# Performance work log

Hardware: AMD Instinct MI355X
Metric: run time of the kernel (lower is better)

The kernel has to match this reference:

```python
import jax, jax.numpy as jnp
import numpy as np

EPSILON = 1e-5  # parameters.EPSILON
BN_EPS = 1e-5
N_NODES, N_EDGES, D = 50000, 400000, 128


def batch_norm(x, gamma, beta):
    # BatchNorm1d in training mode: biased batch statistics over dim 0
    m = jnp.mean(x, axis=0)
    v = jnp.var(x, axis=0)
    return (x - m) * jax.lax.rsqrt(v + BN_EPS) * gamma + beta


def setup_inputs() -> dict:
    key = jax.random.key(0)
    ks = jax.random.split(key, 16)
    s = 0.05
    d = D
    inp = {
        "h": jax.random.normal(ks[0], (N_NODES, d), jnp.float32),
        "e": jax.random.normal(ks[1], (N_EDGES, d), jnp.float32),
        "src": jax.random.randint(ks[2], (N_EDGES,), 0, N_NODES, jnp.int32),
        "dst": jax.random.randint(ks[3], (N_EDGES,), 0, N_NODES, jnp.int32),
        # weights stored [in, out]
        "W_emb_node": jax.random.normal(ks[4], (d, d)) * s,
        "W_emb_edge": jax.random.normal(ks[5], (d, d)) * s,
        "W_emb_eta": jax.random.normal(ks[6], (d, d)) * s,
        "Uw": jax.random.normal(ks[7], (d, d)) * s, "Ub": jnp.zeros((d,)),
        "Vw": jax.random.normal(ks[8], (d, d)) * s, "Vb": jnp.zeros((d,)),
        "W1w": jax.random.normal(ks[9], (d, d)) * s, "W1b": jnp.zeros((d,)),
        "W2w": jax.random.normal(ks[10], (d, d)) * s, "W2b": jnp.zeros((d,)),
        "W3w": jax.random.normal(ks[11], (d, d)) * s, "W3b": jnp.zeros((d,)),
        "h_gamma": jnp.ones((d,)), "h_beta": jnp.zeros((d,)),
        "e_gamma": jnp.ones((d,)), "e_beta": jnp.zeros((d,)),
    }
    return inp


def reference(h, e, src, dst, W_emb_node, W_emb_edge, W_emb_eta,
              Uw, Ub, Vw, Vb, W1w, W1b, W2w, W2b, W3w, W3b,
              h_gamma, h_beta, e_gamma, e_beta):
    n_nodes = h.shape[0]
    # node-level linear projections
    h_emb = h @ W_emb_node                 # [N, d]
    Uh = h @ Uw + Ub                       # [N, d]
    Vh = h @ Vw + Vb                       # [N, d]
    W2h = h @ W2w + W2b                    # [N, d]
    W3h = h @ W3w + W3b                    # [N, d]
    # edge-level
    e_emb = e @ W_emb_edge                 # [E, d]
    W1e = e @ W1w + W1b                    # [E, d]
    # edge update: e_ij = emb(e) + ReLU(BN(W1 e + W2 h_src + W3 h_dst))
    pre_e = W1e + W2h[src] + W3h[dst]      # gather [E, d]
    e_new = e_emb + jax.nn.relu(batch_norm(pre_e, e_gamma, e_beta))
    # gate: sigma_ij = embedding_eta(sigmoid(e_ij))
    sigma = jax.nn.sigmoid(e_new) @ W_emb_eta  # [E, d]
    # weighted-sum aggregation to destination nodes
    num = jax.ops.segment_sum(sigma * Vh[src], dst, num_segments=n_nodes)
    den = jax.ops.segment_sum(sigma, dst, num_segments=n_nodes)
    agg = num / (den + EPSILON)            # [N, d]
    h_new = h_emb + jax.nn.relu(batch_norm(Uh + agg, h_gamma, h_beta))
    return (h_new, e_new)
```

## Files before the change

kernel.cpp:

```cpp
#include <hip/hip_runtime.h>
#include <cstdint>
#include <cstddef>
#include <cmath>

#define DD 128

typedef short bf16x8 __attribute__((ext_vector_type(8)));
typedef float f32x4 __attribute__((ext_vector_type(4)));

static __device__ __forceinline__ short f2bf(float f){
  union { float f; uint32_t u; } v; v.f = f;
  uint32_t r = v.u + 0x7FFFu + ((v.u >> 16) & 1u);
  return (short)(r >> 16);
}
static __device__ __forceinline__ float bf2f(short h){
  union { uint32_t u; float f; } v; v.u = ((uint32_t)(uint16_t)h) << 16;
  return v.f;
}
static __device__ __forceinline__ double shfl_xor_f64(double v, int m){
  long long l = __double_as_longlong(v);
  int lo = (int)(l & 0xffffffffLL);
  int hi = (int)((unsigned long long)l >> 32);
  lo = __shfl_xor(lo, m, 64);
  hi = __shfl_xor(hi, m, 64);
  return __longlong_as_double(((long long)hi << 32) | (unsigned long long)(unsigned int)lo);
}

template<int EP>
__global__ __launch_bounds__(256, 2) void fgemm_k(
    const float* __restrict__ X, const float* __restrict__ W,
    const float* __restrict__ bias, float* __restrict__ Y,
    int M, int nTiles,
    const int* __restrict__ src, const int* __restrict__ dst,
    const float* __restrict__ T2, const float* __restrict__ T3,
    const float* __restrict__ mF, const float* __restrict__ rF,
    const float* __restrict__ gammaF, const float* __restrict__ betaF,
    double* __restrict__ eSum, double* __restrict__ eSumSq)
{
  __shared__ float sA[128][68];
  __shared__ float sW[64][128];
  __shared__ double redS[(EP == 1) ? 4 : 1][32][4];
  __shared__ double redQ[(EP == 1) ? 4 : 1][32][4];

  const int tid = threadIdx.x;
  const int tx = tid & 31;
  const int ty = tid >> 5;
  const int c0 = tx * 4;
  const int r0 = ty * 16;
  const int lane = tid & 63, wv = tid >> 6;

  float bias_c[4];
  #pragma unroll
  for (int j = 0; j < 4; ++j) bias_c[j] = bias ? bias[c0 + j] : 0.0f;

  double st_s[4] = {0,0,0,0}, st_q[4] = {0,0,0,0};

  for (int tile = blockIdx.x; tile < nTiles; tile += gridDim.x){
    const int rowBase = tile * 128;
    float acc[16][4];
    #pragma unroll
    for (int r = 0; r < 16; ++r)
      #pragma unroll
      for (int j = 0; j < 4; ++j) acc[r][j] = 0.0f;

    #pragma unroll
    for (int h = 0; h < 2; ++h){
      {
        int kk = ty * 8;
        #pragma unroll
        for (int q = 0; q < 8; ++q)
          *(f32x4*)&sW[kk + q][c0] = *(const f32x4*)&W[(size_t)(h*64 + kk + q) * DD + c0];
      }
      {
        int r = tid >> 1;
        int koff = (tid & 1) * 32;
        int ar = rowBase + r; if (ar >= M) ar = M - 1;
        const float* xp = X + (size_t)ar * DD + h*64 + koff;
        #pragma unroll
        for (int q = 0; q < 8; ++q){
          f32x4 v = *(const f32x4*)(xp + q * 4);
          if (EP == 3){
            #pragma unroll
            for (int j = 0; j < 4; ++j) v[j] = 1.0f / (1.0f + expf(-v[j]));
          }
          *(f32x4*)&sA[r][koff + q * 4] = v;
        }
      }
      __syncthreads();

      #pragma unroll 2
      for (int q = 0; q < 16; ++q){
        f32x4 b0 = *(const f32x4*)&sW[4*q + 0][c0];
        f32x4 b1 = *(const f32x4*)&sW[4*q + 1][c0];
        f32x4 b2 = *(const f32x4*)&sW[4*q + 2][c0];
        f32x4 b3 = *(const f32x4*)&sW[4*q + 3][c0];
        #pragma unroll
        for (int r = 0; r < 16; ++r){
          f32x4 a = *(const f32x4*)&sA[r0 + r][4*q];
          #pragma unroll
          for (int j = 0; j < 4; ++j){
            acc[r][j] = fmaf(a[0], b0[j], acc[r][j]);
            acc[r][j] = fmaf(a[1], b1[j], acc[r][j]);
            acc[r][j] = fmaf(a[2], b2[j], acc[r][j]);
            acc[r][j] = fmaf(a[3], b3[j], acc[r][j]);
          }
        }
      }
      __syncthreads();
    }

    #pragma unroll
    for (int r = 0; r < 16; ++r){
      int row = rowBase + r0 + r;
      if (row < M){
        size_t base = (size_t)row * DD + c0;
        if (EP == 0){
          f32x4 o;
          #pragma unroll
          for (int j = 0; j < 4; ++j) o[j] = acc[r][j] + bias_c[j];
          *(f32x4*)&Y[base] = o;
        } else if (EP == 1){
          int s = src[row], d = dst[row];
          f32x4 t2 = *(const f32x4*)&T2[(size_t)s * DD + c0];
          f32x4 t3 = *(const f32x4*)&T3[(size_t)d * DD + c0];
          f32x4 o;
          #pragma unroll
          for (int j = 0; j < 4; ++j){
            o[j] = ((acc[r][j] + bias_c[j]) + t2[j]) + t3[j];
            st_s[j] += (double)o[j];
            st_q[j] += (double)o[j] * (double)o[j];
          }
          *(f32x4*)&Y[base] = o;
        } else if (EP == 2){
          f32x4 pe = *(const f32x4*)&Y[base];
          f32x4 o;
          #pragma unroll
          for (int j = 0; j < 4; ++j){
            float xm  = pe[j] - mF[c0 + j];
            float t1  = xm * rF[c0 + j];
            float t2v = t1 * gammaF[c0 + j];
            float t3v = t2v + betaF[c0 + j];
            float t = fmaxf(t3v, 0.0f);
            o[j] = acc[r][j] + t;
          }
          *(f32x4*)&Y[base] = o;
        } else {
          f32x4 o;
          #pragma unroll
          for (int j = 0; j < 4; ++j) o[j] = acc[r][j];
          *(f32x4*)&Y[base] = o;
        }
      }
    }
  }

  if (EP == 1){
    #pragma unroll
    for (int j = 0; j < 4; ++j){
      st_s[j] += shfl_xor_f64(st_s[j], 32);
      st_q[j] += shfl_xor_f64(st_q[j], 32);
    }
    if (lane < 32){
      #pragma unroll
      for (int j = 0; j < 4; ++j){ redS[wv][lane][j] = st_s[j]; redQ[wv][lane][j] = st_q[j]; }
    }
    __syncthreads();
    if (tid < 128){
      int txx = tid >> 2, j = tid & 3;
      double s = 0.0, q = 0.0;
      #pragma unroll
      for (int w = 0; w < 4; ++w){ s += redS[w][txx][j]; q += redQ[w][txx][j]; }
      atomicAdd(&eSum[txx*4 + j], s);
      atomicAdd(&eSumSq[txx*4 + j], q);
    }
  }
}

__global__ void hist_k(const int* __restrict__ dst, int NE, int* __restrict__ counts){
  int i = blockIdx.x * blockDim.x + threadIdx.x;
  if (i < NE) atomicAdd(&counts[dst[i]], 1);
}

__global__ __launch_bounds__(1024, 1) void scan_k(const int* __restrict__ counts, int NN,
                                                  int* __restrict__ rowStart, int* __restrict__ cursor){
  __shared__ int part[1024];
  const int T = 1024, t = threadIdx.x;
  const int chunk = (NN + T - 1) / T;
  const int lo = t * chunk;
  const int hi = (lo + chunk < NN) ? lo + chunk : NN;
  int s = 0;
  for (int i = lo; i < hi; ++i) s += counts[i];
  part[t] = s;
  __syncthreads();
  for (int off = 1; off < T; off <<= 1){
    int v = (t >= off) ? part[t - off] : 0;
    __syncthreads();
    part[t] += v;
    __syncthreads();
  }
  int run = (t == 0) ? 0 : part[t - 1];
  for (int i = lo; i < hi; ++i){ rowStart[i] = run; cursor[i] = run; run += counts[i]; }
  if (t == T - 1) rowStart[NN] = run;
}

__global__ void place_k(const int* __restrict__ dst, int NE,
                        int* __restrict__ cursor, int* __restrict__ edgeIdx){
  int i = blockIdx.x * blockDim.x + threadIdx.x;
  if (i < NE){ int p = atomicAdd(&cursor[dst[i]], 1); edgeIdx[p] = i; }
}

__global__ __launch_bounds__(256, 4) void gather_k(
    const float* __restrict__ sigma, const float* __restrict__ Vh,
    const int* __restrict__ rowStart, const int* __restrict__ edgeIdx,
    const int* __restrict__ srcArr,
    const float* __restrict__ Uh, float* __restrict__ preH, int NN)
{
  const int lane = threadIdx.x & 63, wv = threadIdx.x >> 6;
  for (int node = blockIdx.x * 4 + wv; node < NN; node += gridDim.x * 4){
    const int beg = rowStart[node], end = rowStart[node + 1];
    float den0 = 0.f, den1 = 0.f, num0 = 0.f, num1 = 0.f;
    for (int eb = beg; eb < end; eb += 4){
      const int nE = end - eb;
      float sg0[4], sg1[4], vh0[4], vh1[4];
      #pragma unroll
      for (int q = 0; q < 4; ++q){
        if (q < nE){
          int eid = edgeIdx[eb + q];
          int s = srcArr[eid];
          sg0[q] = sigma[(size_t)eid * DD + lane];
          sg1[q] = sigma[(size_t)eid * DD + 64 + lane];
          vh0[q] = Vh[(size_t)s * DD + lane];
          vh1[q] = Vh[(size_t)s * DD + 64 + lane];
        } else { sg0[q] = 0.f; sg1[q] = 0.f; vh0[q] = 0.f; vh1[q] = 0.f; }
      }
      #pragma unroll
      for (int q = 0; q < 4; ++q){
        den0 += sg0[q]; den1 += sg1[q];
        num0 = fmaf(sg0[q], vh0[q], num0);
        num1 = fmaf(sg1[q], vh1[q], num1);
      }
    }
    const size_t b = (size_t)node * DD;
    preH[b + lane]      = Uh[b + lane]      + num0 / (den0 + 1e-5f);
    preH[b + 64 + lane] = Uh[b + 64 + lane] + num1 / (den1 + 1e-5f);
  }
}

__global__ void finalizeE_k(const double* __restrict__ sum, const double* __restrict__ sumsq,
                            double M, float* __restrict__ mF, float* __restrict__ rF)
{
  int c = threadIdx.x;
  double m = sum[c] / M;
  double v = sumsq[c] / M - m * m;
  float vf = (float)v;
  mF[c] = (float)m;
  rF[c] = 1.0f / sqrtf(vf + 1e-5f);
}

__global__ void stats64_k(const float* __restrict__ X, int M,
                          double* __restrict__ sum, double* __restrict__ sumsq)
{
  const int col = threadIdx.x & 127;
  const int half = threadIdx.x >> 7;
  double s = 0.0, q = 0.0;
  for (int r = blockIdx.x * 2 + half; r < M; r += gridDim.x * 2){
    double v = (double)X[(size_t)r * DD + col];
    s += v; q += v * v;
  }
  __shared__ double sS[256], sQ[256];
  sS[threadIdx.x] = s; sQ[threadIdx.x] = q;
  __syncthreads();
  if (half == 0){
    atomicAdd(&sum[col],   sS[col] + sS[col + 128]);
    atomicAdd(&sumsq[col], sQ[col] + sQ[col + 128]);
  }
}

__global__ void finalize64_k(const double* __restrict__ sum, const double* __restrict__ sumsq,
                             double M, const float* __restrict__ gamma, const float* __restrict__ beta,
                             double* __restrict__ scale, double* __restrict__ shift)
{
  int c = threadIdx.x;
  double m = sum[c] / M;
  double var = sumsq[c] / M - m * m;
  double sc = (double)gamma[c] / sqrt(var + 1e-5);
  scale[c] = sc;
  shift[c] = (double)beta[c] - m * sc;
}

__global__ __launch_bounds__(256, 2) void hfinal_mfma_k(
    const float* __restrict__ X, const float* __restrict__ W,
    float* __restrict__ Y, int M, int rowTiles,
    const float* __restrict__ preH,
    const double* __restrict__ hSc, const double* __restrict__ hSh)
{
  const int tid = threadIdx.x;
  const int lane = tid & 63;
  const int wv = tid >> 6;
  const int l15 = lane & 15;
  const int lg = lane >> 4;
  const int colBase = blockIdx.y * 64;

  __shared__ short sW[2][64][136];
  for (int t = tid; t < 64 * 128; t += 256){
    int k = t >> 6, nl = t & 63;
    float w = W[k * DD + colBase + nl];
    short hi = f2bf(w);
    sW[0][nl][k] = hi;
    sW[1][nl][k] = f2bf(w - bf2f(hi));
  }
  __syncthreads();

  bf16x8 Bhi[4][4], Blo[4][4];
  #pragma unroll
  for (int ct = 0; ct < 4; ++ct)
    #pragma unroll
    for (int ks = 0; ks < 4; ++ks){
      Bhi[ct][ks] = *(const bf16x8*)&sW[0][ct*16 + l15][ks*32 + lg*8];
      Blo[ct][ks] = *(const bf16x8*)&sW[1][ct*16 + l15][ks*32 + lg*8];
    }

  for (int rt = blockIdx.x; rt < rowTiles; rt += gridDim.x){
    int arow = rt * 64 + wv * 16 + l15;
    if (arow >= M) arow = M - 1;
    const f32x4* xr = (const f32x4*)(X + (size_t)arow * DD);

    bf16x8 Ahi[4], Alo[4];
    #pragma unroll
    for (int ks = 0; ks < 4; ++ks){
      f32x4 a0 = xr[ks*8 + lg*2];
      f32x4 a1 = xr[ks*8 + lg*2 + 1];
      float av[8];
      #pragma unroll
      for (int j = 0; j < 4; ++j){ av[j] = a0[j]; av[4+j] = a1[j]; }
      #pragma unroll
      for (int j = 0; j < 8; ++j){
        short hi = f2bf(av[j]);
        Ahi[ks][j] = hi;
        Alo[ks][j] = f2bf(av[j] - bf2f(hi));
      }
    }

    f32x4 acc[4];
    #pragma unroll
    for (int ct = 0; ct < 4; ++ct) acc[ct] = (f32x4){0.f, 0.f, 0.f, 0.f};
    #pragma unroll
    for (int ct = 0; ct < 4; ++ct)
      #pragma unroll
      for (int ks = 0; ks < 4; ++ks){
        acc[ct] = __builtin_amdgcn_mfma_f32_16x16x32_bf16(Ahi[ks], Bhi[ct][ks], acc[ct], 0, 0, 0);
        acc[ct] = __builtin_amdgcn_mfma_f32_16x16x32_bf16(Ahi[ks], Blo[ct][ks], acc[ct], 0, 0, 0);
        acc[ct] = __builtin_amdgcn_mfma_f32_16x16x32_bf16(Alo[ks], Bhi[ct][ks], acc[ct], 0, 0, 0);
      }

    const int r0 = rt * 64 + wv * 16 + lg * 4;
    #pragma unroll
    for (int reg = 0; reg < 4; ++reg){
      int r = r0 + reg;
      if (r < M){
        #pragma unroll
        for (int ct = 0; ct < 4; ++ct){
          int c = colBase + ct*16 + l15;
          double t = (double)preH[(size_t)r * DD + c] * hSc[c] + hSh[c];
          float tv = t > 0.0 ? (float)t : 0.0f;
          Y[(size_t)r * DD + c] = acc[ct][reg] + tv;
        }
      }
    }
  }
}

extern "C" void kernel_launch(void* const* d_in, const int* in_sizes, int n_in,
                              void* d_out, int out_size, void* d_ws, size_t ws_size,
                              hipStream_t stream)
{
  const float* h  = (const float*)d_in[0];
  const float* e  = (const float*)d_in[1];
  const int* src  = (const int*)d_in[2];
  const int* dst  = (const int*)d_in[3];
  const float* Wemb_n   = (const float*)d_in[4];
  const float* Wemb_e   = (const float*)d_in[5];
  const float* Wemb_eta = (const float*)d_in[6];
  const float* Uw  = (const float*)d_in[7];  const float* Ub  = (const float*)d_in[8];
  const float* Vw  = (const float*)d_in[9];  const float* Vb  = (const float*)d_in[10];
  const float* W1w = (const float*)d_in[11]; const float* W1b = (const float*)d_in[12];
  const float* W2w = (const float*)d_in[13]; const float* W2b = (const float*)d_in[14];
  const float* W3w = (const float*)d_in[15]; const float* W3b = (const float*)d_in[16];
  const float* h_gamma = (const float*)d_in[17]; const float* h_beta = (const float*)d_in[18];
  const float* e_gamma = (const float*)d_in[19]; const float* e_beta = (const float*)d_in[20];

  const int NN = in_sizes[0] / DD;
  const int NE = in_sizes[2];

  char* wsp = (char*)d_ws;
  float* W2h   = (float*)wsp;  wsp += (size_t)NN * DD * sizeof(float);
  float* W3h   = (float*)wsp;  wsp += (size_t)NN * DD * sizeof(float);
  float* Vh    = (float*)wsp;  wsp += (size_t)NN * DD * sizeof(float);
  float* sigma = (float*)wsp;  wsp += (size_t)NE * DD * sizeof(float);
  double* stats = (double*)wsp; wsp += 6 * DD * sizeof(double);
  double* eSum = stats;        double* eSumSq = stats + DD;
  double* hSum = stats + 2*DD; double* hSumSq = stats + 3*DD;
  double* hScale = stats + 4*DD; double* hShift = stats + 5*DD;
  float* mF = (float*)wsp;   wsp += DD * sizeof(float);
  float* rF = (float*)wsp;   wsp += DD * sizeof(float);
  int* counts   = (int*)wsp; wsp += (size_t)NN * sizeof(int);
  int* rowStart = (int*)wsp; wsp += ((size_t)NN + 1) * sizeof(int);
  int* cursor   = (int*)wsp; wsp += (size_t)NN * sizeof(int);
  int* edgeIdx  = (int*)wsp; wsp += (size_t)NE * sizeof(int);

  float* h_new_out = (float*)d_out;
  float* e_out     = (float*)d_out + (size_t)NN * DD;

  const int tN = (NN + 127) / 128;
  const int tE = (NE + 127) / 128;
  const int rtN64 = (NN + 63) / 64;
  dim3 blk(256);

  hipMemsetAsync(stats, 0, (size_t)4 * DD * sizeof(double), stream);
  hipMemsetAsync(counts, 0, (size_t)NN * sizeof(int), stream);

  hist_k<<<(NE + 255) / 256, blk, 0, stream>>>(dst, NE, counts);
  scan_k<<<1, 1024, 0, stream>>>(counts, NN, rowStart, cursor);
  place_k<<<(NE + 255) / 256, blk, 0, stream>>>(dst, NE, cursor, edgeIdx);

  fgemm_k<0><<<tN, blk, 0, stream>>>(h, Uw, Ub, h_new_out, NN, tN,
      nullptr,nullptr,nullptr,nullptr,nullptr,nullptr,nullptr,nullptr,nullptr,nullptr);
  fgemm_k<0><<<tN, blk, 0, stream>>>(h, Vw, Vb, Vh, NN, tN,
      nullptr,nullptr,nullptr,nullptr,nullptr,nullptr,nullptr,nullptr,nullptr,nullptr);
  fgemm_k<0><<<tN, blk, 0, stream>>>(h, W2w, W2b, W2h, NN, tN,
      nullptr,nullptr,nullptr,nullptr,nullptr,nullptr,nullptr,nullptr,nullptr,nullptr);
  fgemm_k<0><<<tN, blk, 0, stream>>>(h, W3w, W3b, W3h, NN, tN,
      nullptr,nullptr,nullptr,nullptr,nullptr,nullptr,nullptr,nullptr,nullptr,nullptr);

  fgemm_k<1><<<1024, blk, 0, stream>>>(e, W1w, W1b, e_out, NE, tE,
      src, dst, W2h, W3h, nullptr,nullptr,nullptr,nullptr, eSum, eSumSq);

  finalizeE_k<<<1, 128, 0, stream>>>(eSum, eSumSq, (double)NE, mF, rF);

  fgemm_k<2><<<tE, blk, 0, stream>>>(e, Wemb_e, nullptr, e_out, NE, tE,
      nullptr,nullptr,nullptr,nullptr, mF, rF, e_gamma, e_beta, nullptr,nullptr);

  fgemm_k<3><<<tE, blk, 0, stream>>>(e_out, Wemb_eta, nullptr, sigma, NE, tE,
      nullptr,nullptr,nullptr,nullptr,nullptr,nullptr,nullptr,nullptr,nullptr,nullptr);

  gather_k<<<(NN + 3) / 4, blk, 0, stream>>>(sigma, Vh, rowStart, edgeIdx, src,
      h_new_out, h_new_out, NN);

  stats64_k<<<512, blk, 0, stream>>>(h_new_out, NN, hSum, hSumSq);
  finalize64_k<<<1, 128, 0, stream>>>(hSum, hSumSq, (double)NN, h_gamma, h_beta, hScale, hShift);

  hfinal_mfma_k<<<dim3(rtN64, 2), blk, 0, stream>>>(h, Wemb_n, h_new_out, NN, rtN64,
      h_new_out, hScale, hShift);
}
```

Before: 1.223 ms.

## Fuse paired node/edge GEMMs sharing inputs and fold edge BN into sigma GEMM

Node projections are paired into dual-output GEMMs (U+V, W2+W3), so h is read twice instead of four times. The edge W1 and embedding GEMMs now share one pass over e. The edge BN/ReLU/residual epilogue moves into the sigma GEMM's A-tile load, which writes e_new and feeds sigmoid(e_new) straight to the eta GEMM. This removes kernel launches and full passes over the large edge arrays. In exchange the dual kernel holds twice the accumulators, raising register pressure, and the sigma kernel works in place on shared buffers.

```diff
diff --git a/kernel.cpp b/kernel.cpp
--- a/kernel.cpp
+++ b/kernel.cpp
@@ -27,34 +27,156 @@
 }
 
 template<int EP>
-__global__ __launch_bounds__(256, 2) void fgemm_k(
-    const float* __restrict__ X, const float* __restrict__ W,
-    const float* __restrict__ bias, float* __restrict__ Y,
+__global__ __launch_bounds__(256, 2) void dgemm_k(
+    const float* __restrict__ X,
+    const float* __restrict__ W1, const float* __restrict__ b1,
+    const float* __restrict__ W2, const float* __restrict__ b2,
+    float* __restrict__ Y1, float* __restrict__ Y2,
     int M, int nTiles,
     const int* __restrict__ src, const int* __restrict__ dst,
     const float* __restrict__ T2, const float* __restrict__ T3,
+    double* __restrict__ eSum, double* __restrict__ eSumSq)
+{
+  __shared__ float sA[128][36];
+  __shared__ float sW1[32][128];
+  __shared__ float sW2[32][128];
+  __shared__ double redS[(EP == 1) ? 4 : 1][32][4];
+  __shared__ double redQ[(EP == 1) ? 4 : 1][32][4];
+
+  const int tid = threadIdx.x, tx = tid & 31, ty = tid >> 5;
+  const int c0 = tx * 4, r0 = ty * 16;
+  const int lane = tid & 63, wv = tid >> 6;
+
+  float b1c[4], b2c[4];
+  #pragma unroll
+  for (int j = 0; j < 4; ++j){
+    b1c[j] = b1 ? b1[c0 + j] : 0.0f;
+    b2c[j] = b2 ? b2[c0 + j] : 0.0f;
+  }
+  double st_s[4] = {0,0,0,0}, st_q[4] = {0,0,0,0};
+
+  #pragma unroll 1
+  for (int tile = blockIdx.x; tile < nTiles; tile += gridDim.x){
+    const int rowBase = tile * 128;
+    float acc1[16][4], acc2[16][4];
+    #pragma unroll
+    for (int r = 0; r < 16; ++r)
+      #pragma unroll
+      for (int j = 0; j < 4; ++j){ acc1[r][j] = 0.0f; acc2[r][j] = 0.0f; }
+
+    #pragma unroll 1
+    for (int h = 0; h < 4; ++h){
+      #pragma unroll
+      for (int m = 0; m < 4; ++m){
+        int k = ty + 8 * m;
+        *(f32x4*)&sW1[k][c0] = *(const f32x4*)&W1[(size_t)(h*32 + k) * DD + c0];
+        *(f32x4*)&sW2[k][c0] = *(const f32x4*)&W2[(size_t)(h*32 + k) * DD + c0];
+      }
+      {
+        int r = tid >> 1, koff = (tid & 1) * 16;
+        int ar = rowBase + r; if (ar >= M) ar = M - 1;
+        const float* xp = X + (size_t)ar * DD + h*32 + koff;
+        #pragma unroll
+        for (int q = 0; q < 4; ++q)
+          *(f32x4*)&sA[r][koff + q*4] = *(const f32x4*)(xp + q*4);
+      }
+      __syncthreads();
+
+      #pragma unroll
+      for (int q = 0; q < 8; ++q){
+        f32x4 wA0 = *(const f32x4*)&sW1[4*q + 0][c0];
+        f32x4 wA1 = *(const f32x4*)&sW1[4*q + 1][c0];
+        f32x4 wA2 = *(const f32x4*)&sW1[4*q + 2][c0];
+        f32x4 wA3 = *(const f32x4*)&sW1[4*q + 3][c0];
+        f32x4 wB0 = *(const f32x4*)&sW2[4*q + 0][c0];
+        f32x4 wB1 = *(const f32x4*)&sW2[4*q + 1][c0];
+        f32x4 wB2 = *(const f32x4*)&sW2[4*q + 2][c0];
+        f32x4 wB3 = *(const f32x4*)&sW2[4*q + 3][c0];
+        #pragma unroll
+        for (int r = 0; r < 16; ++r){
+          f32x4 a = *(const f32x4*)&sA[r0 + r][4*q];
+          #pragma unroll
+          for (int j = 0; j < 4; ++j){
+            float t1 = acc1[r][j];
+            t1 = fmaf(a[0], wA0[j], t1); t1 = fmaf(a[1], wA1[j], t1);
+            t1 = fmaf(a[2], wA2[j], t1); t1 = fmaf(a[3], wA3[j], t1);
+            acc1[r][j] = t1;
+            float t2 = acc2[r][j];
+            t2 = fmaf(a[0], wB0[j], t2); t2 = fmaf(a[1], wB1[j], t2);
+            t2 = fmaf(a[2], wB2[j], t2); t2 = fmaf(a[3], wB3[j], t2);
+            acc2[r][j] = t2;
+          }
+        }
+      }
+      __syncthreads();
+    }
+
+    #pragma unroll
+    for (int r = 0; r < 16; ++r){
+      int row = rowBase + r0 + r;
+      if (row < M){
+        size_t base = (size_t)row * DD + c0;
+        if (EP == 0){
+          f32x4 o1, o2;
+          #pragma unroll
+          for (int j = 0; j < 4; ++j){ o1[j] = acc1[r][j] + b1c[j]; o2[j] = acc2[r][j] + b2c[j]; }
+          *(f32x4*)&Y1[base] = o1;
+          *(f32x4*)&Y2[base] = o2;
+        } else {
+          int s = src[row], d = dst[row];
+          f32x4 t2v = *(const f32x4*)&T2[(size_t)s * DD + c0];
+          f32x4 t3v = *(const f32x4*)&T3[(size_t)d * DD + c0];
+          f32x4 o1, o2;
+          #pragma unroll
+          for (int j = 0; j < 4; ++j){
+            o1[j] = ((acc1[r][j] + b1c[j]) + t2v[j]) + t3v[j];
+            st_s[j] += (double)o1[j];
+            st_q[j] += (double)o1[j] * (double)o1[j];
+            o2[j] = acc2[r][j];
+          }
+          *(f32x4*)&Y1[base] = o1;
+          *(f32x4*)&Y2[base] = o2;
+        }
+      }
+    }
+  }
+
+  if (EP == 1){
+    #pragma unroll
+    for (int j = 0; j < 4; ++j){
+      st_s[j] += shfl_xor_f64(st_s[j], 32);
+      st_q[j] += shfl_xor_f64(st_q[j], 32);
+    }
+    if (lane < 32){
+      #pragma unroll
+      for (int j = 0; j < 4; ++j){ redS[wv][lane][j] = st_s[j]; redQ[wv][lane][j] = st_q[j]; }
+    }
+    __syncthreads();
+    if (tid < 128){
+      int txx = tid >> 2, j = tid & 3;
+      double s = 0.0, q = 0.0;
+      #pragma unroll
+      for (int w = 0; w < 4; ++w){ s += redS[w][txx][j]; q += redQ[w][txx][j]; }
+      atomicAdd(&eSum[txx*4 + j], s);
+      atomicAdd(&eSumSq[txx*4 + j], q);
+    }
+  }
+}
+
+__global__ __launch_bounds__(256, 2) void sgemm_k(
+    const float* __restrict__ preE, const float* __restrict__ eEmb,
+    const float* __restrict__ Weta,
+    float* __restrict__ eNew, float* __restrict__ sigmaOut,
     const float* __restrict__ mF, const float* __restrict__ rF,
-    const float* __restrict__ gammaF, const float* __restrict__ betaF,
-    double* __restrict__ eSum, double* __restrict__ eSumSq)
+    const float* __restrict__ gF, const float* __restrict__ bF,
+    int M, int nTiles)
 {
   __shared__ float sA[128][68];
   __shared__ float sW[64][128];
-  __shared__ double redS[(EP == 1) ? 4 : 1][32][4];
-  __shared__ double redQ[(EP == 1) ? 4 : 1][32][4];
-
-  const int tid = threadIdx.x;
-  const int tx = tid & 31;
-  const int ty = tid >> 5;
-  const int c0 = tx * 4;
-  const int r0 = ty * 16;
-  const int lane = tid & 63, wv = tid >> 6;
-
-  float bias_c[4];
-  #pragma unroll
-  for (int j = 0; j < 4; ++j) bias_c[j] = bias ? bias[c0 + j] : 0.0f;
-
-  double st_s[4] = {0,0,0,0}, st_q[4] = {0,0,0,0};
-
+  const int tid = threadIdx.x, tx = tid & 31, ty = tid >> 5;
+  const int c0 = tx * 4, r0 = ty * 16;
+
+  #pragma unroll 1
   for (int tile = blockIdx.x; tile < nTiles; tile += gridDim.x){
     const int rowBase = tile * 128;
     float acc[16][4];
@@ -63,27 +185,42 @@
       #pragma unroll
       for (int j = 0; j < 4; ++j) acc[r][j] = 0.0f;
 
-    #pragma unroll
+    #pragma unroll 1
     for (int h = 0; h < 2; ++h){
       {
         int kk = ty * 8;
         #pragma unroll
         for (int q = 0; q < 8; ++q)
-          *(f32x4*)&sW[kk + q][c0] = *(const f32x4*)&W[(size_t)(h*64 + kk + q) * DD + c0];
+          *(f32x4*)&sW[kk + q][c0] = *(const f32x4*)&Weta[(size_t)(h*64 + kk + q) * DD + c0];
       }
       {
-        int r = tid >> 1;
-        int koff = (tid & 1) * 32;
-        int ar = rowBase + r; if (ar >= M) ar = M - 1;
-        const float* xp = X + (size_t)ar * DD + h*64 + koff;
+        int r = tid >> 1, koff = (tid & 1) * 32;
+        int ar = rowBase + r;
+        int gcb = h*64 + koff;
+        const float* pp = preE + (size_t)ar * DD + gcb;
+        const float* ep = eEmb + (size_t)ar * DD + gcb;
+        float* np = eNew + (size_t)ar * DD + gcb;
         #pragma unroll
         for (int q = 0; q < 8; ++q){
-          f32x4 v = *(const f32x4*)(xp + q * 4);
-          if (EP == 3){
-            #pragma unroll
-            for (int j = 0; j < 4; ++j) v[j] = 1.0f / (1.0f + expf(-v[j]));
+          f32x4 pe = *(const f32x4*)(pp + q*4);
+          f32x4 em = *(const f32x4*)(ep + q*4);
+          f32x4 mm = *(const f32x4*)&mF[gcb + q*4];
+          f32x4 rr = *(const f32x4*)&rF[gcb + q*4];
+          f32x4 gg = *(const f32x4*)&gF[gcb + q*4];
+          f32x4 bb = *(const f32x4*)&bF[gcb + q*4];
+          f32x4 en, sg;
+          #pragma unroll
+          for (int j = 0; j < 4; ++j){
+            float xm  = pe[j] - mm[j];
+            float t1  = xm * rr[j];
+            float t2v = t1 * gg[j];
+            float t3v = t2v + bb[j];
+            float t = fmaxf(t3v, 0.0f);
+            en[j] = em[j] + t;
+            sg[j] = 1.0f / (1.0f + expf(-en[j]));
           }
-          *(f32x4*)&sA[r][koff + q * 4] = v;
+          *(f32x4*)(np + q*4) = en;
+          *(f32x4*)&sA[r][koff + q*4] = sg;
         }
       }
       __syncthreads();
@@ -99,10 +236,10 @@
           f32x4 a = *(const f32x4*)&sA[r0 + r][4*q];
           #pragma unroll
           for (int j = 0; j < 4; ++j){
-            acc[r][j] = fmaf(a[0], b0[j], acc[r][j]);
-            acc[r][j] = fmaf(a[1], b1[j], acc[r][j]);
-            acc[r][j] = fmaf(a[2], b2[j], acc[r][j]);
-            acc[r][j] = fmaf(a[3], b3[j], acc[r][j]);
+            float t = acc[r][j];
+            t = fmaf(a[0], b0[j], t); t = fmaf(a[1], b1[j], t);
+            t = fmaf(a[2], b2[j], t); t = fmaf(a[3], b3[j], t);
+            acc[r][j] = t;
           }
         }
       }
@@ -112,66 +249,10 @@
     #pragma unroll
     for (int r = 0; r < 16; ++r){
       int row = rowBase + r0 + r;
-      if (row < M){
-        size_t base = (size_t)row * DD + c0;
-        if (EP == 0){
-          f32x4 o;
-          #pragma unroll
-          for (int j = 0; j < 4; ++j) o[j] = acc[r][j] + bias_c[j];
-          *(f32x4*)&Y[base] = o;
-        } else if (EP == 1){
-          int s = src[row], d = dst[row];
-          f32x4 t2 = *(const f32x4*)&T2[(size_t)s * DD + c0];
-          f32x4 t3 = *(const f32x4*)&T3[(size_t)d * DD + c0];
-          f32x4 o;
-          #pragma unroll
-          for (int j = 0; j < 4; ++j){
-            o[j] = ((acc[r][j] + bias_c[j]) + t2[j]) + t3[j];
-            st_s[j] += (double)o[j];
-            st_q[j] += (double)o[j] * (double)o[j];
-          }
-          *(f32x4*)&Y[base] = o;
-        } else if (EP == 2){
-          f32x4 pe = *(const f32x4*)&Y[base];
-          f32x4 o;
-          #pragma unroll
-          for (int j = 0; j < 4; ++j){
-            float xm  = pe[j] - mF[c0 + j];
-            float t1  = xm * rF[c0 + j];
-            float t2v = t1 * gammaF[c0 + j];
-            float t3v = t2v + betaF[c0 + j];
-            float t = fmaxf(t3v, 0.0f);
-            o[j] = acc[r][j] + t;
-          }
-          *(f32x4*)&Y[base] = o;
-        } else {
-          f32x4 o;
-          #pragma unroll
-          for (int j = 0; j < 4; ++j) o[j] = acc[r][j];
-          *(f32x4*)&Y[base] = o;
-        }
-      }
-    }
-  }
-
-  if (EP == 1){
-    #pragma unroll
-    for (int j = 0; j < 4; ++j){
-      st_s[j] += shfl_xor_f64(st_s[j], 32);
-      st_q[j] += shfl_xor_f64(st_q[j], 32);
-    }
-    if (lane < 32){
-      #pragma unroll
-      for (int j = 0; j < 4; ++j){ redS[wv][lane][j] = st_s[j]; redQ[wv][lane][j] = st_q[j]; }
-    }
-    __syncthreads();
-    if (tid < 128){
-      int txx = tid >> 2, j = tid & 3;
-      double s = 0.0, q = 0.0;
-      #pragma unroll
-      for (int w = 0; w < 4; ++w){ s += redS[w][txx][j]; q += redQ[w][txx][j]; }
-      atomicAdd(&eSum[txx*4 + j], s);
-      atomicAdd(&eSumSq[txx*4 + j], q);
+      f32x4 o;
+      #pragma unroll
+      for (int j = 0; j < 4; ++j) o[j] = acc[r][j];
+      *(f32x4*)&sigmaOut[(size_t)row * DD + c0] = o;
     }
   }
 }
@@ -393,10 +474,10 @@
   const int NE = in_sizes[2];
 
   char* wsp = (char*)d_ws;
-  float* W2h   = (float*)wsp;  wsp += (size_t)NN * DD * sizeof(float);
-  float* W3h   = (float*)wsp;  wsp += (size_t)NN * DD * sizeof(float);
-  float* Vh    = (float*)wsp;  wsp += (size_t)NN * DD * sizeof(float);
-  float* sigma = (float*)wsp;  wsp += (size_t)NE * DD * sizeof(float);
+  float* W2h    = (float*)wsp;  wsp += (size_t)NN * DD * sizeof(float);
+  float* W3h    = (float*)wsp;  wsp += (size_t)NN * DD * sizeof(float);
+  float* Vh     = (float*)wsp;  wsp += (size_t)NN * DD * sizeof(float);
+  float* embSig = (float*)wsp;  wsp += (size_t)NE * DD * sizeof(float);
   double* stats = (double*)wsp; wsp += 6 * DD * sizeof(double);
   double* eSum = stats;        double* eSumSq = stats + DD;
   double* hSum = stats + 2*DD; double* hSumSq = stats + 3*DD;
@@ -423,27 +504,20 @@
   scan_k<<<1, 1024, 0, stream>>>(counts, NN, rowStart, cursor);
   place_k<<<(NE + 255) / 256, blk, 0, stream>>>(dst, NE, cursor, edgeIdx);
 
-  fgemm_k<0><<<tN, blk, 0, stream>>>(h, Uw, Ub, h_new_out, NN, tN,
-      nullptr,nullptr,nullptr,nullptr,nullptr,nullptr,nullptr,nullptr,nullptr,nullptr);
-  fgemm_k<0><<<tN, blk, 0, stream>>>(h, Vw, Vb, Vh, NN, tN,
-      nullptr,nullptr,nullptr,nullptr,nullptr,nullptr,nullptr,nullptr,nullptr,nullptr);
-  fgemm_k<0><<<tN, blk, 0, stream>>>(h, W2w, W2b, W2h, NN, tN,
-      nullptr,nullptr,nullptr,nullptr,nullptr,nullptr,nullptr,nullptr,nullptr,nullptr);
-  fgemm_k<0><<<tN, blk, 0, stream>>>(h, W3w, W3b, W3h, NN, tN,
-      nullptr,nullptr,nullptr,nullptr,nullptr,nullptr,nullptr,nullptr,nullptr,nullptr);
-
-  fgemm_k<1><<<1024, blk, 0, stream>>>(e, W1w, W1b, e_out, NE, tE,
-      src, dst, W2h, W3h, nullptr,nullptr,nullptr,nullptr, eSum, eSumSq);
+  dgemm_k<0><<<tN, blk, 0, stream>>>(h, Uw, Ub, Vw, Vb, h_new_out, Vh, NN, tN,
+      nullptr, nullptr, nullptr, nullptr, nullptr, nullptr);
+  dgemm_k<0><<<tN, blk, 0, stream>>>(h, W2w, W2b, W3w, W3b, W2h, W3h, NN, tN,
+      nullptr, nullptr, nullptr, nullptr, nullptr, nullptr);
+
+  dgemm_k<1><<<1024, blk, 0, stream>>>(e, W1w, W1b, Wemb_e, nullptr, e_out, embSig,
+      NE, tE, src, dst, W2h, W3h, eSum, eSumSq);
 
   finalizeE_k<<<1, 128, 0, stream>>>(eSum, eSumSq, (double)NE, mF, rF);
 
-  fgemm_k<2><<<tE, blk, 0, stream>>>(e, Wemb_e, nullptr, e_out, NE, tE,
-      nullptr,nullptr,nullptr,nullptr, mF, rF, e_gamma, e_beta, nullptr,nullptr);
-
-  fgemm_k<3><<<tE, blk, 0, stream>>>(e_out, Wemb_eta, nullptr, sigma, NE, tE,
-      nullptr,nullptr,nullptr,nullptr,nullptr,nullptr,nullptr,nullptr,nullptr,nullptr);
-
-  gather_k<<<(NN + 3) / 4, blk, 0, stream>>>(sigma, Vh, rowStart, edgeIdx, src,
+  sgemm_k<<<tE, blk, 0, stream>>>(e_out, embSig, Wemb_eta, e_out, embSig,
+      mF, rF, e_gamma, e_beta, NE, tE);
+
+  gather_k<<<(NN + 3) / 4, blk, 0, stream>>>(embSig, Vh, rowStart, edgeIdx, src,
       h_new_out, h_new_out, NN);
 
   stats64_k<<<512, blk, 0, stream>>>(h_new_out, NN, hSum, hSumSq);
```

New measurement: 1.251 ms. +2.3%, slower.
